# Kernel tuning notes

Hardware: AMD Instinct MI355X
Metric: run time of the kernel (lower is better)

## Reference

```python
import jax, jax.numpy as jnp
import numpy as np

B, S, V, E, H, DM = 4, 512, 32000, 512, 1024, 256
U, M = 4096, 1024
MEM_CAP = 512 * 4  # max_length * memory_segments


def setup_inputs() -> dict:
    key = jax.random.key(0)
    ks = jax.random.split(key, 26)
    def n(k, shape, s=0.02):
        return jax.random.normal(k, shape, dtype=jnp.float32) * s
    return {
        'input_ids': jax.random.randint(ks[0], (B, S), 0, V),
        'past_tokens': jax.random.randint(ks[1], (B, M), 0, V),
        'past_keys': jax.random.normal(ks[2], (B, M, DM), dtype=jnp.float32),
        'untied_ids': jax.random.randint(ks[3], (U,), 0, V),
        'emb': n(ks[4], (V, E)),
        'gru_w_ih': n(ks[5], (3 * H, E)), 'gru_w_hh': n(ks[6], (3 * H, H)),
        'gru_b_ih': n(ks[7], (3 * H,)), 'gru_b_hh': n(ks[8], (3 * H,)),
        'q_w': n(ks[9], (DM, H)), 'q_b': n(ks[10], (DM,)),
        'k_w': n(ks[11], (DM, H)), 'k_b': n(ks[12], (DM,)),
        'gate_w': n(ks[13], (1, H)), 'gate_b': n(ks[14], (1,)),
        'fc_w': n(ks[15], (4 * E, H)), 'fc_b': n(ks[16], (4 * E,)),
        'proj_w': n(ks[17], (E, 4 * E)), 'proj_b': n(ks[18], (E,)),
        'out_bias': jnp.zeros((V,), jnp.float32),
        'part_w': n(ks[19], (U, E)), 'part_b': n(ks[20], (U,)),
        'mem_scale': jnp.float32(6.0),
    }


def _gru(x, w_ih, w_hh, b_ih, b_hh):
    # x: [B,S,E] -> states [B,S,H]; torch GRU cell math
    xp = x @ w_ih.T + b_ih  # [B,S,3H]
    h0 = jnp.zeros((x.shape[0], w_hh.shape[1]), x.dtype)
    def step(h, xp_t):
        hp = h @ w_hh.T + b_hh
        xr, xz, xn = jnp.split(xp_t, 3, axis=-1)
        hr, hz, hn = jnp.split(hp, 3, axis=-1)
        r = jax.nn.sigmoid(xr + hr)
        z = jax.nn.sigmoid(xz + hz)
        nn_ = jnp.tanh(xn + r * hn)
        h_new = (1.0 - z) * nn_ + z * h
        return h_new, h_new
    h_last, states = jax.lax.scan(step, h0, jnp.swapaxes(xp, 0, 1))
    return jnp.swapaxes(states, 0, 1), h_last


def reference(input_ids, past_tokens, past_keys, untied_ids, emb,
              gru_w_ih, gru_w_hh, gru_b_ih, gru_b_hh,
              q_w, q_b, k_w, k_b, gate_w, gate_b,
              fc_w, fc_b, proj_w, proj_b, out_bias, part_w, part_b, mem_scale):
    x = emb[input_ids]                                  # [B,S,E]
    states, _ = _gru(x, gru_w_ih, gru_w_hh, gru_b_ih, gru_b_hh)  # dropout=eval identity
    head = jnp.square(jax.nn.relu(states @ fc_w.T + fc_b))       # [B,S,4E]
    base = head @ proj_w.T + proj_b                                # [B,S,E]
    logits = base @ emb.T + out_bias                               # [B,S,V]
    partial = base @ part_w.T + part_b                             # [B,S,U]
    logits = logits.at[:, :, untied_ids].add(partial)              # scatter_add over vocab

    q = states @ q_w.T + q_b                                       # [B,S,DM]
    ck = states @ k_w.T + k_b                                      # [B,S,DM]
    scale = jnp.float32(1.0 / np.sqrt(DM))
    cur_scores = jnp.einsum('bsd,btd->bst', q, ck) * scale
    causal = jnp.tril(jnp.ones((S, S), bool), k=-1)                # strictly-past mask
    neg = jnp.finfo(cur_scores.dtype).min
    masked_cur = jnp.where(causal[None], cur_scores, neg)
    past_scores = jnp.einsum('bsd,bmd->bsm', q, past_keys) * scale
    all_scores = jnp.concatenate([past_scores, masked_cur], axis=-1)   # [B,S,M+S]
    all_mask = jnp.concatenate([
        jnp.ones((B, S, M), bool),
        jnp.broadcast_to(causal[None], (B, S, S))], axis=-1)
    att = jax.nn.softmax(all_scores, axis=-1) * all_mask
    att = att / jnp.maximum(att.sum(axis=-1, keepdims=True), 1e-6)
    val_idx = jnp.concatenate([
        jnp.broadcast_to(past_tokens[:, None, :], (B, S, M)),
        jnp.broadcast_to(input_ids[:, None, :], (B, S, S))], axis=-1)   # [B,S,M+S]
    gate = jax.nn.sigmoid(states @ gate_w.T + gate_b)               # [B,S,1]
    gated = att * (gate * mem_scale)
    b_idx = jnp.arange(B)[:, None, None]
    s_idx = jnp.arange(S)[None, :, None]
    logits = logits.at[b_idx, s_idx, val_idx].add(gated)            # irregular scatter_add

    next_keys = jax.lax.stop_gradient(
        jnp.concatenate([past_keys, ck], axis=1))[:, -MEM_CAP:]
    next_tokens = jnp.concatenate([past_tokens, input_ids], axis=1)[:, -MEM_CAP:]
    return logits, next_keys, next_tokens
```

## Files before the change

kernel.cpp:

```cpp
#include <hip/hip_runtime.h>
#include <cstddef>
#include <cstring>

#define BB 4
#define SS 512
#define VV 32000
#define EE 512
#define HH 1024
#define DM 256
#define UU 4096
#define MM 1024
#define TT 1536

typedef __attribute__((ext_vector_type(8))) short short8v;
typedef __attribute__((ext_vector_type(4))) float f32x4;

__device__ __forceinline__ unsigned long long agent_ld64(const unsigned long long* p) {
  return __hip_atomic_load(const_cast<unsigned long long*>(p), __ATOMIC_RELAXED,
                           __HIP_MEMORY_SCOPE_AGENT);
}
__device__ __forceinline__ void agent_st64(unsigned long long* p, unsigned long long v) {
  __hip_atomic_store(p, v, __ATOMIC_RELAXED, __HIP_MEMORY_SCOPE_AGENT);
}
__device__ __forceinline__ float sigmoidf_(float x) { return 1.f / (1.f + __expf(-x)); }

__device__ __forceinline__ unsigned short f2bf_rtn(float x) {
  unsigned u; __builtin_memcpy(&u, &x, 4);
  unsigned r = (u + 0x7FFFu + ((u >> 16) & 1u)) >> 16;
  return (unsigned short)r;
}
__device__ __forceinline__ float bf2f(unsigned short b) {
  unsigned u = ((unsigned)b) << 16; float f; __builtin_memcpy(&f, &u, 4); return f;
}

__global__ __launch_bounds__(256) void split_bf16(
    const float* __restrict__ in, unsigned short* __restrict__ hi,
    unsigned short* __restrict__ lo, int n)
{
  for (int i = blockIdx.x * 256 + threadIdx.x; i < n; i += gridDim.x * 256) {
    float x = in[i];
    unsigned short h = f2bf_rtn(x);
    hi[i] = h;
    lo[i] = f2bf_rtn(x - bf2f(h));
  }
}

__global__ __launch_bounds__(256) void gemm_mfma_bt(
    const unsigned short* __restrict__ Ah, const unsigned short* __restrict__ Al,
    const int* __restrict__ a_idx,
    const unsigned short* __restrict__ Wh, const unsigned short* __restrict__ Wl,
    const float* __restrict__ bias, float* __restrict__ C, int K, int ldc,
    int act, const int* __restrict__ sidx)
{
  const int tid = threadIdx.x, lane = tid & 63, w = tid >> 6;
  const int bm = blockIdx.y * 128, bn = blockIdx.x * 128;
  const int wm = (w >> 1) * 64, wn = (w & 1) * 64;
  const int r = lane & 15, ko = (lane >> 4) * 8;

  int arow[4];
#pragma unroll
  for (int mi = 0; mi < 4; ++mi) {
    int row = bm + wm + mi * 16 + r;
    arow[mi] = a_idx ? a_idx[row] : row;
  }

  f32x4 acc[4][4] = {};

  for (int k0 = 0; k0 < K; k0 += 32) {
    short8v ah[4], al[4], bh[4], bl[4];
#pragma unroll
    for (int mi = 0; mi < 4; ++mi) {
      size_t off = (size_t)arow[mi] * K + k0 + ko;
      ah[mi] = *(const short8v*)(Ah + off);
      al[mi] = *(const short8v*)(Al + off);
    }
#pragma unroll
    for (int ni = 0; ni < 4; ++ni) {
      size_t off = (size_t)(bn + wn + ni * 16 + r) * K + k0 + ko;
      bh[ni] = *(const short8v*)(Wh + off);
      bl[ni] = *(const short8v*)(Wl + off);
    }
#pragma unroll
    for (int mi = 0; mi < 4; ++mi)
#pragma unroll
      for (int ni = 0; ni < 4; ++ni) {
        acc[mi][ni] = __builtin_amdgcn_mfma_f32_16x16x32_bf16(ah[mi], bh[ni], acc[mi][ni], 0, 0, 0);
        acc[mi][ni] = __builtin_amdgcn_mfma_f32_16x16x32_bf16(ah[mi], bl[ni], acc[mi][ni], 0, 0, 0);
        acc[mi][ni] = __builtin_amdgcn_mfma_f32_16x16x32_bf16(al[mi], bh[ni], acc[mi][ni], 0, 0, 0);
      }
  }

#pragma unroll
  for (int mi = 0; mi < 4; ++mi)
#pragma unroll
    for (int ni = 0; ni < 4; ++ni) {
      const int row = bm + wm + mi * 16 + (lane >> 4) * 4;
      const int col = bn + wn + ni * 16 + (lane & 15);
      const float bv = bias[col];
      const int scol = sidx ? sidx[col] : col;
#pragma unroll
      for (int i = 0; i < 4; ++i) {
        float v = acc[mi][ni][i] + bv;
        if (act == 1) { v = fmaxf(v, 0.f); v *= v; }
        if (sidx) atomicAdd(C + (size_t)(row + i) * ldc + scol, v);
        else      C[(size_t)(row + i) * ldc + scol] = v;
      }
    }
}

template <int TILE, int MICRO>
__global__ __launch_bounds__(256) void gemm_k(
    const float* __restrict__ A, const int* __restrict__ a_idx,
    const float* __restrict__ W, const float* __restrict__ bias,
    float* __restrict__ C, int K, int ldc, int act, const int* __restrict__ sidx)
{
  constexpr int PITCH = TILE + 4;
  __shared__ float As[16][PITCH];
  __shared__ float Ws[16][PITCH];
  const int tid = threadIdx.x;
  const int bm = blockIdx.y * TILE, bn = blockIdx.x * TILE;
  const int tr = tid >> 4, tc = tid & 15;
  const int lk = tid & 15, lr0 = tid >> 4;
  float acc[MICRO][MICRO] = {};

  for (int k0 = 0; k0 < K; k0 += 16) {
#pragma unroll
    for (int jj = 0; jj < TILE / 16; ++jj) {
      int row = lr0 + (jj << 4);
      int am = bm + row;
      int ar = a_idx ? a_idx[am] : am;
      As[lk][row] = A[(size_t)ar * K + k0 + lk];
      Ws[lk][row] = W[(size_t)(bn + row) * K + k0 + lk];
    }
    __syncthreads();
#pragma unroll
    for (int kk = 0; kk < 16; ++kk) {
      float av[MICRO], wv[MICRO];
#pragma unroll
      for (int i = 0; i < MICRO; ++i) av[i] = As[kk][tr * MICRO + i];
#pragma unroll
      for (int j = 0; j < MICRO; ++j) wv[j] = Ws[kk][tc * MICRO + j];
#pragma unroll
      for (int i = 0; i < MICRO; ++i)
#pragma unroll
        for (int j = 0; j < MICRO; ++j) acc[i][j] += av[i] * wv[j];
    }
    __syncthreads();
  }

#pragma unroll
  for (int i = 0; i < MICRO; ++i) {
    int m = bm + tr * MICRO + i;
    float tmp[MICRO];
#pragma unroll
    for (int j = 0; j < MICRO; ++j) {
      int n = bn + tc * MICRO + j;
      float v = acc[i][j] + bias[n];
      if (act == 1) { v = fmaxf(v, 0.f); v *= v; }
      tmp[j] = v;
    }
    if (sidx) {
#pragma unroll
      for (int j = 0; j < MICRO; ++j)
        atomicAdd(C + (size_t)m * ldc + sidx[bn + tc * MICRO + j], tmp[j]);
    } else {
      float* cp = C + (size_t)m * ldc + bn + tc * MICRO;
#pragma unroll
      for (int j4 = 0; j4 < MICRO / 4; ++j4)
        *(float4*)(cp + 4 * j4) =
            make_float4(tmp[4 * j4], tmp[4 * j4 + 1], tmp[4 * j4 + 2], tmp[4 * j4 + 3]);
    }
  }
}

__global__ __launch_bounds__(512, 1) void gru_scan(
    const float* __restrict__ xp,
    const float* __restrict__ w_hh,
    const float* __restrict__ b_hh,
    float* __restrict__ states,
    unsigned long long* hbuf)
{
  __shared__ float h_lds[2][HH];
  const int tid = threadIdx.x;
  const int lane = tid & 63;
  const int wv = tid >> 6;
  const int bb = blockIdx.x >> 5;
  const int r = blockIdx.x & 31;
  const int c0 = (r << 5) + (wv << 2);

  unsigned long long* hb = hbuf + ((size_t)bb << 11);

  float wreg[4][3][16];
#pragma unroll
  for (int k = 0; k < 4; ++k)
#pragma unroll
    for (int g = 0; g < 3; ++g) {
      const float* wr = w_hh + (size_t)((g << 10) + c0 + k) * HH + lane;
#pragma unroll
      for (int i = 0; i < 16; ++i) wreg[k][g][i] = wr[i << 6];
    }
  float bh[4][3];
#pragma unroll
  for (int k = 0; k < 4; ++k)
#pragma unroll
    for (int g = 0; g < 3; ++g) bh[k][g] = b_hh[(g << 10) + c0 + k];

  for (int i = tid; i < HH; i += 512) h_lds[0][i] = 0.f;
  __syncthreads();

  for (int t = 0; t < SS; ++t) {
    const int cur = t & 1, nxt = (t + 1) & 1;
    const float* hc = h_lds[cur];

    float4 xrv, xzv, xnv, hold;
    if (lane == 0) {
      const float* xpr = xp + (size_t)((bb << 9) + t) * 3072 + c0;
      xrv = *(const float4*)(xpr);
      xzv = *(const float4*)(xpr + HH);
      xnv = *(const float4*)(xpr + 2 * HH);
      hold = *(const float4*)(hc + c0);
    }

    float acc[4][3] = {};
#pragma unroll
    for (int i = 0; i < 16; ++i) {
      float hv = hc[(i << 6) + lane];
#pragma unroll
      for (int k = 0; k < 4; ++k) {
        acc[k][0] += hv * wreg[k][0][i];
        acc[k][1] += hv * wreg[k][1][i];
        acc[k][2] += hv * wreg[k][2][i];
      }
    }
#pragma unroll
    for (int off = 32; off >= 1; off >>= 1)
#pragma unroll
      for (int k = 0; k < 4; ++k) {
        acc[k][0] += __shfl_xor(acc[k][0], off, 64);
        acc[k][1] += __shfl_xor(acc[k][1], off, 64);
        acc[k][2] += __shfl_xor(acc[k][2], off, 64);
      }

    if (lane == 0) {
      const unsigned long long tagw = ((unsigned long long)(unsigned)(t + 1)) << 32;
      float xr[4] = {xrv.x, xrv.y, xrv.z, xrv.w};
      float xz[4] = {xzv.x, xzv.y, xzv.z, xzv.w};
      float xn[4] = {xnv.x, xnv.y, xnv.z, xnv.w};
      float ho[4] = {hold.x, hold.y, hold.z, hold.w};
      float hv4[4];
#pragma unroll
      for (int k = 0; k < 4; ++k) {
        float rr = sigmoidf_(xr[k] + acc[k][0] + bh[k][0]);
        float zz = sigmoidf_(xz[k] + acc[k][1] + bh[k][1]);
        float nn = tanhf(xn[k] + rr * (acc[k][2] + bh[k][2]));
        hv4[k] = (1.f - zz) * nn + zz * ho[k];
      }
      if (t < SS - 1) {
        unsigned long long* dst = hb + ((size_t)nxt << 10) + c0;
#pragma unroll
        for (int k = 0; k < 4; ++k) {
          unsigned hbits;
          __builtin_memcpy(&hbits, &hv4[k], 4);
          agent_st64(dst + k, tagw | (unsigned long long)hbits);
        }
      }
      *(float4*)(states + (size_t)((bb << 9) + t) * HH + c0) =
          make_float4(hv4[0], hv4[1], hv4[2], hv4[3]);
    }
    if (t == SS - 1) break;

    {
      const unsigned tgt = (unsigned)(t + 1);
      const unsigned long long* src = hb + ((size_t)nxt << 10) + (tid << 1);
      unsigned long long p0, p1;
      for (;;) {
        p0 = agent_ld64(src);
        p1 = agent_ld64(src + 1);
        if ((unsigned)(p0 >> 32) >= tgt && (unsigned)(p1 >> 32) >= tgt) break;
      }
      h_lds[nxt][(tid << 1)] = __uint_as_float((unsigned)p0);
      h_lds[nxt][(tid << 1) + 1] = __uint_as_float((unsigned)p1);
    }
    __syncthreads();
  }
}

__global__ __launch_bounds__(256) void gate_kernel(
    const float* __restrict__ states, const float* __restrict__ gate_w,
    const float* __restrict__ gate_b, float* __restrict__ out)
{
  const int lane = threadIdx.x & 63;
  const int row = (blockIdx.x << 2) + (threadIdx.x >> 6);
  float s = 0.f;
#pragma unroll
  for (int i = 0; i < 16; ++i)
    s += states[(size_t)row * HH + (i << 6) + lane] * gate_w[(i << 6) + lane];
#pragma unroll
  for (int off = 32; off >= 1; off >>= 1) s += __shfl_xor(s, off, 64);
  if (lane == 0) out[row] = sigmoidf_(s + gate_b[0]);
}

__global__ __launch_bounds__(256) void copy_next(
    const float* __restrict__ past_keys, const float* __restrict__ ck,
    const int* __restrict__ past_tokens, const int* __restrict__ input_ids,
    float* __restrict__ nk, float* __restrict__ ntokf)
{
  const int i = blockIdx.x * 256 + threadIdx.x;
  if (i < BB * TT * 64) {
    int b = i / (TT * 64);
    int rem = i - b * (TT * 64);
    int t = rem >> 6, c = rem & 63;
    float4 v;
    if (t < MM) v = ((const float4*)past_keys)[((b << 10) + t) * 64 + c];
    else        v = ((const float4*)ck)[((b << 9) + (t - MM)) * 64 + c];
    ((float4*)nk)[i] = v;
  }
  if (i < BB * TT) {
    int b = i / TT, t = i - b * TT;
    int tok = (t < MM) ? past_tokens[(b << 10) + t] : input_ids[(b << 9) + t - MM];
    ntokf[i] = (float)tok;
  }
}

__global__ __launch_bounds__(256) void attn_scatter(
    const float* __restrict__ qbuf,
    const float* __restrict__ nk,
    const float* __restrict__ ntokf,
    const float* __restrict__ gate,
    const float* __restrict__ msp,
    float* __restrict__ logits)
{
  __shared__ float q_s[8][260];
  __shared__ float k_s[32][260];
  const int b = blockIdx.y;
  const int s0 = blockIdx.x << 3;
  const int tid = threadIdx.x, lane = tid & 63, wv = tid >> 6;
  const int half = lane >> 5, tl = lane & 31;
  const int ss = wv + (half << 2);
  const int sg = s0 + ss;
  const int limit = MM + sg;

  for (int i = tid; i < 8 * 256; i += 256)
    q_s[i >> 8][i & 255] = qbuf[(size_t)((b << 9) + s0 + (i >> 8)) * DM + (i & 255)];

  const int kr = tid >> 3, kc = (tid & 7) << 5;
  float mx = -1e30f, sum = 0.f;
  float fscale = 0.f;

  for (int pass = 0; pass < 2; ++pass) {
    if (pass == 1) {
#pragma unroll
      for (int off = 16; off >= 1; off >>= 1) {
        float mo = __shfl_xor(mx, off, 64);
        float so = __shfl_xor(sum, off, 64);
        float m2 = fmaxf(mx, mo);
        sum = sum * __expf(mx - m2) + so * __expf(mo - m2);
        mx = m2;
      }
      fscale = gate[(b << 9) + sg] * msp[0] / sum;
    }
    for (int tile = 0; tile < 48; ++tile) {
      __syncthreads();
      {
        const float4* src = (const float4*)(nk + ((size_t)(b * TT + (tile << 5) + kr) << 8) + kc);
        float4* dst = (float4*)(&k_s[kr][kc]);
#pragma unroll
        for (int u = 0; u < 8; ++u) dst[u] = src[u];
      }
      __syncthreads();
      int t = (tile << 5) + tl;
      if (t < limit) {
        float a = 0.f;
#pragma unroll 8
        for (int d = 0; d < 256; d += 4) {
          float4 kv = *(const float4*)&k_s[tl][d];
          float4 qv = *(const float4*)&q_s[ss][d];
          a += kv.x * qv.x + kv.y * qv.y + kv.z * qv.z + kv.w * qv.w;
        }
        a *= 0.0625f;
        if (pass == 0) {
          float m2 = fmaxf(mx, a);
          sum = sum * __expf(mx - m2) + __expf(a - m2);
          mx = m2;
        } else {
          int tok = (int)ntokf[b * TT + t];
          atomicAdd(logits + (size_t)((b << 9) + sg) * VV + tok,
                    __expf(a - mx) * fscale);
        }
      }
    }
  }
}

extern "C" void kernel_launch(void* const* d_in, const int* in_sizes, int n_in,
                              void* d_out, int out_size, void* d_ws, size_t ws_size,
                              hipStream_t stream) {
  (void)in_sizes; (void)n_in; (void)out_size;
  const int*   input_ids   = (const int*)  d_in[0];
  const int*   past_tokens = (const int*)  d_in[1];
  const float* past_keys   = (const float*)d_in[2];
  const int*   untied_ids  = (const int*)  d_in[3];
  const float* emb         = (const float*)d_in[4];
  const float* w_ih        = (const float*)d_in[5];
  const float* w_hh        = (const float*)d_in[6];
  const float* b_ih        = (const float*)d_in[7];
  const float* b_hh        = (const float*)d_in[8];
  const float* q_w         = (const float*)d_in[9];
  const float* q_b         = (const float*)d_in[10];
  const float* k_w         = (const float*)d_in[11];
  const float* k_b         = (const float*)d_in[12];
  const float* gate_w      = (const float*)d_in[13];
  const float* gate_b      = (const float*)d_in[14];
  const float* fc_w        = (const float*)d_in[15];
  const float* fc_b        = (const float*)d_in[16];
  const float* proj_w      = (const float*)d_in[17];
  const float* proj_b      = (const float*)d_in[18];
  const float* out_bias    = (const float*)d_in[19];
  const float* part_w      = (const float*)d_in[20];
  const float* part_b      = (const float*)d_in[21];
  const float* mem_scale   = (const float*)d_in[22];

  char* ws = (char*)d_ws;
  unsigned long long* hbuf = (unsigned long long*)(ws + 4096);
  float* gatebuf  = (float*)(ws + 69632);
  float* qb       = (float*)(ws + 81920);
  float* ckb      = (float*)(ws + 2179072);
  float* xp       = (float*)(ws + 4276224);
  float* states   = (float*)(ws + 29442048);
  float* head     = (float*)(ws + 37830656);
  float* base     = (float*)(ws + 54607872);
  unsigned short* embh    = (unsigned short*)(ws + 58802176);
  unsigned short* embl    = (unsigned short*)(ws + 91570176);
  unsigned short* baseh   = (unsigned short*)(ws + 124338176);
  unsigned short* basel   = (unsigned short*)(ws + 126435328);
  const bool use_mfma = ws_size >= 128532480ull;
  unsigned short* w_ihh   = (unsigned short*)(ws + 128532480);
  unsigned short* w_ihl   = (unsigned short*)(ws + 131678208);
  unsigned short* fc_wh   = (unsigned short*)(ws + 134823936);
  unsigned short* fc_wl   = (unsigned short*)(ws + 139018240);
  unsigned short* proj_wh = (unsigned short*)(ws + 143212544);
  unsigned short* proj_wl = (unsigned short*)(ws + 145309696);
  unsigned short* part_wh = (unsigned short*)(ws + 147406848);
  unsigned short* part_wl = (unsigned short*)(ws + 151601152);
  unsigned short* statesh = (unsigned short*)(ws + 155795456);
  unsigned short* statesl = (unsigned short*)(ws + 159989760);
  unsigned short* headh   = (unsigned short*)(ws + 164184064);
  unsigned short* headl   = (unsigned short*)(ws + 172572672);
  const bool use_mfma2 = ws_size >= 180961280ull;

  float* logits = (float*)d_out;
  float* nk     = logits + 65536000ll;
  float* ntokf  = logits + 67108864ll;

  hipMemsetAsync(ws, 0, 69632, stream);

  if (use_mfma)
    split_bf16<<<2048, 256, 0, stream>>>(emb, embh, embl, VV * EE);
  if (use_mfma2) {
    split_bf16<<<512, 256, 0, stream>>>(w_ih, w_ihh, w_ihl, 3072 * EE);
    split_bf16<<<512, 256, 0, stream>>>(fc_w, fc_wh, fc_wl, 2048 * HH);
    split_bf16<<<512, 256, 0, stream>>>(proj_w, proj_wh, proj_wl, EE * 2048);
    split_bf16<<<512, 256, 0, stream>>>(part_w, part_wh, part_wl, UU * EE);
  }

  if (use_mfma2)
    gemm_mfma_bt<<<dim3(3072 / 128, 2048 / 128), 256, 0, stream>>>(
        embh, embl, input_ids, w_ihh, w_ihl, b_ih, xp, EE, 3072, 0, nullptr);
  else
    gemm_k<128, 8><<<dim3(3072 / 128, 2048 / 128), 256, 0, stream>>>(
        emb, input_ids, w_ih, b_ih, xp, EE, 3072, 0, nullptr);

  gru_scan<<<128, 512, 0, stream>>>(xp, w_hh, b_hh, states, hbuf);

  if (use_mfma2) {
    split_bf16<<<512, 256, 0, stream>>>(states, statesh, statesl, 2048 * HH);
    gemm_mfma_bt<<<dim3(2048 / 128, 2048 / 128), 256, 0, stream>>>(
        statesh, statesl, nullptr, fc_wh, fc_wl, fc_b, head, HH, 2048, 1, nullptr);
  } else {
    gemm_k<128, 8><<<dim3(2048 / 128, 2048 / 128), 256, 0, stream>>>(
        states, nullptr, fc_w, fc_b, head, HH, 2048, 1, nullptr);
  }

  if (use_mfma2) {
    split_bf16<<<1024, 256, 0, stream>>>(head, headh, headl, 2048 * 2048);
    gemm_mfma_bt<<<dim3(512 / 128, 2048 / 128), 256, 0, stream>>>(
        headh, headl, nullptr, proj_wh, proj_wl, proj_b, base, 2048, EE, 0, nullptr);
  } else {
    gemm_k<64, 4><<<dim3(512 / 64, 2048 / 64), 256, 0, stream>>>(
        head, nullptr, proj_w, proj_b, base, 2048, EE, 0, nullptr);
  }

  if (use_mfma) {
    split_bf16<<<512, 256, 0, stream>>>(base, baseh, basel, 2048 * EE);
    gemm_mfma_bt<<<dim3(VV / 128, 2048 / 128), 256, 0, stream>>>(
        baseh, basel, nullptr, embh, embl, out_bias, logits, EE, VV, 0, nullptr);
  } else {
    gemm_k<128, 8><<<dim3(VV / 128, 2048 / 128), 256, 0, stream>>>(
        base, nullptr, emb, out_bias, logits, EE, VV, 0, nullptr);
  }

  if (use_mfma2)
    gemm_mfma_bt<<<dim3(UU / 128, 2048 / 128), 256, 0, stream>>>(
        baseh, basel, nullptr, part_wh, part_wl, part_b, logits, EE, VV, 0, untied_ids);
  else
    gemm_k<128, 8><<<dim3(UU / 128, 2048 / 128), 256, 0, stream>>>(
        base, nullptr, part_w, part_b, logits, EE, VV, 0, untied_ids);

  gemm_k<64, 4><<<dim3(DM / 64, 2048 / 64), 256, 0, stream>>>(
      states, nullptr, q_w, q_b, qb, HH, DM, 0, nullptr);
  gemm_k<64, 4><<<dim3(DM / 64, 2048 / 64), 256, 0, stream>>>(
      states, nullptr, k_w, k_b, ckb, HH, DM, 0, nullptr);

  gate_kernel<<<512, 256, 0, stream>>>(states, gate_w, gate_b, gatebuf);

  copy_next<<<1536, 256, 0, stream>>>(past_keys, ckb, past_tokens, input_ids, nk, ntokf);

  attn_scatter<<<dim3(SS / 8, BB), 256, 0, stream>>>(qb, nk, ntokf, gatebuf, mem_scale, logits);
}
```

Baseline: 5.257 ms.

## Compute attention scores with split-bf16 MFMA and separate softmax-scatter kernel

Replaces the fused attention-scatter kernel with three stages. Query and key buffers are split into bf16 hi/lo pairs, the score matrix is computed with 3-term MFMA into a workspace buffer, and a row-wise softmax kernel then atomically scatters the gated weights into the logits. The aim is to move the QK dot products onto matrix cores. In exchange it adds split passes and a round trip of a 12MB score buffer through memory. It only runs when the workspace is large enough.

```diff
diff --git a/kernel.cpp b/kernel.cpp
--- a/kernel.cpp
+++ b/kernel.cpp
@@ -106,6 +106,102 @@
         else      C[(size_t)(row + i) * ldc + scol] = v;
       }
     }
+}
+
+__global__ __launch_bounds__(256) void score_mfma(
+    const unsigned short* __restrict__ qh, const unsigned short* __restrict__ ql,
+    const unsigned short* __restrict__ kh, const unsigned short* __restrict__ kl,
+    float* __restrict__ scores)
+{
+  const int b = blockIdx.z;
+  const unsigned short* Ah = qh + (size_t)b * SS * DM;
+  const unsigned short* Al = ql + (size_t)b * SS * DM;
+  const unsigned short* Wh = kh + (size_t)b * TT * DM;
+  const unsigned short* Wl = kl + (size_t)b * TT * DM;
+  float* C = scores + (size_t)b * SS * TT;
+
+  const int tid = threadIdx.x, lane = tid & 63, w = tid >> 6;
+  const int bm = blockIdx.y * 128, bn = blockIdx.x * 128;
+  const int wm = (w >> 1) * 64, wn = (w & 1) * 64;
+  const int r = lane & 15, ko = (lane >> 4) * 8;
+
+  f32x4 acc[4][4] = {};
+
+  for (int k0 = 0; k0 < DM; k0 += 32) {
+    short8v ah[4], al[4], bh[4], bl[4];
+#pragma unroll
+    for (int mi = 0; mi < 4; ++mi) {
+      size_t off = (size_t)(bm + wm + mi * 16 + r) * DM + k0 + ko;
+      ah[mi] = *(const short8v*)(Ah + off);
+      al[mi] = *(const short8v*)(Al + off);
+    }
+#pragma unroll
+    for (int ni = 0; ni < 4; ++ni) {
+      size_t off = (size_t)(bn + wn + ni * 16 + r) * DM + k0 + ko;
+      bh[ni] = *(const short8v*)(Wh + off);
+      bl[ni] = *(const short8v*)(Wl + off);
+    }
+#pragma unroll
+    for (int mi = 0; mi < 4; ++mi)
+#pragma unroll
+      for (int ni = 0; ni < 4; ++ni) {
+        acc[mi][ni] = __builtin_amdgcn_mfma_f32_16x16x32_bf16(ah[mi], bh[ni], acc[mi][ni], 0, 0, 0);
+        acc[mi][ni] = __builtin_amdgcn_mfma_f32_16x16x32_bf16(ah[mi], bl[ni], acc[mi][ni], 0, 0, 0);
+        acc[mi][ni] = __builtin_amdgcn_mfma_f32_16x16x32_bf16(al[mi], bh[ni], acc[mi][ni], 0, 0, 0);
+      }
+  }
+
+#pragma unroll
+  for (int mi = 0; mi < 4; ++mi)
+#pragma unroll
+    for (int ni = 0; ni < 4; ++ni) {
+      const int row = bm + wm + mi * 16 + (lane >> 4) * 4;
+      const int col = bn + wn + ni * 16 + (lane & 15);
+#pragma unroll
+      for (int i = 0; i < 4; ++i)
+        C[(size_t)(row + i) * TT + col] = acc[mi][ni][i];
+    }
+}
+
+__global__ __launch_bounds__(256) void softmax_scatter(
+    const float* __restrict__ scores,
+    const float* __restrict__ ntokf,
+    const float* __restrict__ gate,
+    const float* __restrict__ msp,
+    float* __restrict__ logits)
+{
+  const int lane = threadIdx.x & 63;
+  const int row = (blockIdx.x << 2) + (threadIdx.x >> 6);
+  const int b = row >> 9, sg = row & 511;
+  const int limit = MM + sg;
+  const float* sr = scores + (size_t)row * TT;
+
+  float v[24];
+  float mx = -1e30f;
+#pragma unroll
+  for (int i = 0; i < 24; ++i) {
+    int t = (i << 6) + lane;
+    v[i] = (t < limit) ? sr[t] * 0.0625f : -1e30f;
+    mx = fmaxf(mx, v[i]);
+  }
+#pragma unroll
+  for (int off = 32; off >= 1; off >>= 1) mx = fmaxf(mx, __shfl_xor(mx, off, 64));
+
+  float sum = 0.f;
+#pragma unroll
+  for (int i = 0; i < 24; ++i) sum += __expf(v[i] - mx);
+#pragma unroll
+  for (int off = 32; off >= 1; off >>= 1) sum += __shfl_xor(sum, off, 64);
+
+  const float fs = gate[row] * msp[0] / sum;
+  const float* tokr = ntokf + b * TT;
+  float* lrow = logits + (size_t)row * VV;
+#pragma unroll
+  for (int i = 0; i < 24; ++i) {
+    int t = (i << 6) + lane;
+    if (t < limit)
+      atomicAdd(lrow + (int)tokr[t], __expf(v[i] - mx) * fs);
+  }
 }
 
 template <int TILE, int MICRO>
@@ -447,6 +543,12 @@
   unsigned short* headh   = (unsigned short*)(ws + 164184064);
   unsigned short* headl   = (unsigned short*)(ws + 172572672);
   const bool use_mfma2 = ws_size >= 180961280ull;
+  float* scores           = (float*)(ws + 180961280);
+  unsigned short* qbh     = (unsigned short*)(ws + 193544192);
+  unsigned short* qbl     = (unsigned short*)(ws + 194592768);
+  unsigned short* nkh     = (unsigned short*)(ws + 195641344);
+  unsigned short* nkl     = (unsigned short*)(ws + 198787072);
+  const bool use_attn = ws_size >= 201932800ull;
 
   float* logits = (float*)d_out;
   float* nk     = logits + 65536000ll;
@@ -515,5 +617,13 @@
 
   copy_next<<<1536, 256, 0, stream>>>(past_keys, ckb, past_tokens, input_ids, nk, ntokf);
 
-  attn_scatter<<<dim3(SS / 8, BB), 256, 0, stream>>>(qb, nk, ntokf, gatebuf, mem_scale, logits);
-}
+  if (use_attn) {
+    split_bf16<<<256, 256, 0, stream>>>(qb, qbh, qbl, 2048 * DM);
+    split_bf16<<<512, 256, 0, stream>>>(nk, nkh, nkl, BB * TT * DM);
+    score_mfma<<<dim3(TT / 128, SS / 128, BB), 256, 0, stream>>>(
+        qbh, qbl, nkh, nkl, scores);
+    softmax_scatter<<<512, 256, 0, stream>>>(scores, ntokf, gatebuf, mem_scale, logits);
+  } else {
+    attn_scatter<<<dim3(SS / 8, BB), 256, 0, stream>>>(qb, nk, ntokf, gatebuf, mem_scale, logits);
+  }
+}
```

Result: faster. 5.078 ms (-3.4%).
